# Kernel optimization log

Measured on AMD Instinct MI355X. Metric: run time of the kernel, lower is better.

Reference implementation:

```python
import jax, jax.numpy as jnp
import numpy as np

EPS = 1e-5  # torch BatchNorm default eps


def _bn_relu(x, g, b, relu):
    # Training-mode BatchNorm1d over (N, C, L): stats over axes (0, 2).
    m = jnp.mean(x, axis=(0, 2), keepdims=True)
    v = jnp.var(x, axis=(0, 2), keepdims=True)
    y = (x - m) * jax.lax.rsqrt(v + EPS) * g[None, :, None] + b[None, :, None]
    return jax.nn.relu(y) if relu else y


def setup_inputs() -> dict:
    key = jax.random.key(0)
    k0, k1, k2 = jax.random.split(key, 3)
    N, C, H = 256, 512, 64  # batch, channels (inplanes==planes), spatial positions (mask_channel)
    x = jax.random.normal(k0, (N, C, H), dtype=jnp.float32)
    # LocallyConnected2d weights: torch shape (1, out, in, H, 1, k^2=1) -> (out, in, H)
    w1 = jax.random.normal(k1, (C, C, H), dtype=jnp.float32) * 0.02
    w2 = jax.random.normal(k2, (C, C, H), dtype=jnp.float32) * 0.02
    g1 = jnp.ones((C,), jnp.float32)
    b1 = jnp.zeros((C,), jnp.float32)
    g2 = jnp.ones((C,), jnp.float32)
    b2 = jnp.zeros((C,), jnp.float32)
    return {"x": x, "w1": w1, "g1": g1, "b1": b1, "w2": w2, "g2": g2, "b2": b2}


def reference(x, w1, g1, b1, w2, g2, b2):
    # conv1: locally-connected 1x1 -> per-position matmul over channels
    out = jnp.einsum('nch,och->noh', x, w1)          # (N, C, H)
    out = _bn_relu(out, g1, b1, relu=True)
    # conv2
    out = jnp.einsum('nch,och->noh', out, w2)
    out = _bn_relu(out, g2, b2, relu=False)
    # residual add (downsample is None) + final relu
    return jax.nn.relu(out + x)
```

## Files before the change

kernel.cpp:

```cpp
#include <hip/hip_runtime.h>

typedef float  f32x4  __attribute__((ext_vector_type(4)));
typedef __bf16 bf16x8 __attribute__((ext_vector_type(8)));
typedef __bf16 bf16x4 __attribute__((ext_vector_type(4)));
typedef __bf16 bf16x2 __attribute__((ext_vector_type(2)));

#define N_ 256
#define C_ 512
#define H_ 64

__global__ __launch_bounds__(256) void k_prep(const float* __restrict__ x,
                                              const float* __restrict__ w1,
                                              const float* __restrict__ w2,
                                              __bf16* __restrict__ xT,
                                              __bf16* __restrict__ w1T,
                                              __bf16* __restrict__ w2T,
                                              float* __restrict__ stats) {
  __shared__ float tile[64][65];
  const int by = blockIdx.y;
  const int t  = threadIdx.x;
  if (by == 0 && blockIdx.x == 0) {
#pragma unroll
    for (int i = 0; i < 8; ++i) stats[i * 256 + t] = 0.f;
  }
  const float* src;
  __bf16* dst;
  int p, P;
  if (by < 256)      { src = x;  dst = xT;  p = by;       P = 256; }
  else if (by < 768) { src = w1; dst = w1T; p = by - 256; P = 512; }
  else               { src = w2; dst = w2T; p = by - 768; P = 512; }
  const int q0 = blockIdx.x * 64;
  const float* s = src + ((size_t)p * 512 + q0) * 64;
  const int a = t >> 4, b = t & 15;
#pragma unroll
  for (int j = 0; j < 4; ++j) {
    const int qq = j * 16 + a;
    const float4 v = *reinterpret_cast<const float4*>(s + qq * 64 + b * 4);
    tile[qq][b * 4 + 0] = v.x;
    tile[qq][b * 4 + 1] = v.y;
    tile[qq][b * 4 + 2] = v.z;
    tile[qq][b * 4 + 3] = v.w;
  }
  __syncthreads();
#pragma unroll
  for (int j = 0; j < 4; ++j) {
    const int hh = j * 16 + a;
    bf16x4 y;
#pragma unroll
    for (int e = 0; e < 4; ++e) y[e] = (__bf16)tile[b * 4 + e][hh];
    *reinterpret_cast<bf16x4*>(dst + ((size_t)hh * P + p) * 512 + q0 + b * 4) = y;
  }
}

template <bool BN_A>
__global__ __launch_bounds__(256, 2) void k_gemm(
    const __bf16* __restrict__ A,
    const __bf16* __restrict__ B,
    __bf16* __restrict__ Co,
    const float* __restrict__ sum_in, const float* __restrict__ sq_in,
    const float* __restrict__ g, const float* __restrict__ bb,
    float* __restrict__ sum_out, float* __restrict__ sq_out) {
  const int wkid = (blockIdx.x & 7) * 64 + (blockIdx.x >> 3);
  const int h  = wkid >> 3;
  const int tm = (wkid >> 2) & 1, tn = wkid & 3;
  const int m0 = tm * 128, n0 = tn * 128;
  const __bf16* Ah = A + ((size_t)h * N_ + m0) * C_;
  const __bf16* Bh = B + ((size_t)h * C_ + n0) * C_;
  __shared__ __bf16 As[2][128 * 64];
  __shared__ __bf16 Bs[2][128 * 64];
  __shared__ float a_lds[512], c_lds[512];
  const int tid  = threadIdx.x;
  const int lane = tid & 63, wid = tid >> 6;
  const int wr = wid >> 1, wc = wid & 1;
  const int lrow8 = lane >> 3;
  const int swz   = (lane & 7) ^ lrow8;

  if (BN_A) {
#pragma unroll
    for (int ch = tid; ch < 512; ch += 256) {
      const float m    = sum_in[ch] * (1.f / 16384.f);
      const float var  = fmaxf(0.f, sq_in[ch] * (1.f / 16384.f) - m * m);
      const float aa   = g[ch] * rsqrtf(var + 1e-5f);
      a_lds[ch] = aa;
      c_lds[ch] = bb[ch] - m * aa;
    }
    __syncthreads();
  }

  auto stage_b = [&](int buf, int kt) {
#pragma unroll
    for (int i = 0; i < 4; ++i) {
      const int rbase = wid * 32 + i * 8;
      const __bf16* gb = Bh + (size_t)(rbase + lrow8) * C_ + kt * 64 + swz * 8;
      __builtin_amdgcn_global_load_lds(
          (const __attribute__((address_space(1))) void*)gb,
          (__attribute__((address_space(3))) void*)(&Bs[buf][rbase * 64]), 16, 0, 0);
    }
  };
  auto stage_a = [&](int buf, int kt) {
#pragma unroll
    for (int i = 0; i < 4; ++i) {
      const int rbase = wid * 32 + i * 8;
      const __bf16* ga = Ah + (size_t)(rbase + lrow8) * C_ + kt * 64 + swz * 8;
      __builtin_amdgcn_global_load_lds(
          (const __attribute__((address_space(1))) void*)ga,
          (__attribute__((address_space(3))) void*)(&As[buf][rbase * 64]), 16, 0, 0);
    }
  };
  const int lr32 = tid >> 3, cch = tid & 7;
  auto load_a = [&](bf16x8* v, int kt) {
#pragma unroll
    for (int i = 0; i < 4; ++i)
      v[i] = *reinterpret_cast<const bf16x8*>(
          Ah + (size_t)(i * 32 + lr32) * C_ + kt * 64 + cch * 8);
  };
  auto bn_write = [&](const bf16x8* v, int buf, int kt) {
    const int cg = kt * 64 + cch * 8;
    const f32x4 s0 = *reinterpret_cast<const f32x4*>(&a_lds[cg]);
    const f32x4 s1 = *reinterpret_cast<const f32x4*>(&a_lds[cg + 4]);
    const f32x4 h0 = *reinterpret_cast<const f32x4*>(&c_lds[cg]);
    const f32x4 h1 = *reinterpret_cast<const f32x4*>(&c_lds[cg + 4]);
#pragma unroll
    for (int i = 0; i < 4; ++i) {
      const int row = i * 32 + lr32;
      bf16x8 y;
#pragma unroll
      for (int e = 0; e < 4; ++e) {
        y[e]     = (__bf16)fmaxf(0.f, fmaf((float)v[i][e],     s0[e], h0[e]));
        y[e + 4] = (__bf16)fmaxf(0.f, fmaf((float)v[i][e + 4], s1[e], h1[e]));
      }
      const int boff = row * 128 + ((cch * 16) ^ ((row & 7) << 4));
      *reinterpret_cast<bf16x8*>(reinterpret_cast<char*>(&As[buf][0]) + boff) = y;
    }
  };

  f32x4 acc[4][4] = {};
  const int fr = lane & 15, kc = lane >> 4;
  auto compute = [&](int buf) {
#pragma unroll
    for (int kk = 0; kk < 2; ++kk) {
      bf16x8 af[4], bfq[4];
#pragma unroll
      for (int mf = 0; mf < 4; ++mf) {
        const int row  = wr * 64 + mf * 16 + fr;
        const int boff = row * 128 + (((kk * 64 + kc * 16)) ^ ((row & 7) << 4));
        af[mf] = *reinterpret_cast<const bf16x8*>(
            reinterpret_cast<const char*>(&As[buf][0]) + boff);
      }
#pragma unroll
      for (int nf = 0; nf < 4; ++nf) {
        const int row  = wc * 64 + nf * 16 + fr;
        const int boff = row * 128 + (((kk * 64 + kc * 16)) ^ ((row & 7) << 4));
        bfq[nf] = *reinterpret_cast<const bf16x8*>(
            reinterpret_cast<const char*>(&Bs[buf][0]) + boff);
      }
#pragma unroll
      for (int mf = 0; mf < 4; ++mf)
#pragma unroll
        for (int nf = 0; nf < 4; ++nf)
          acc[mf][nf] = __builtin_amdgcn_mfma_f32_16x16x32_bf16(af[mf], bfq[nf], acc[mf][nf], 0, 0, 0);
    }
  };

  if (BN_A) {
    bf16x8 v0[4];
    load_a(v0, 0);
    bn_write(v0, 0, 0);
  } else {
    stage_a(0, 0);
  }
  stage_b(0, 0);
  __syncthreads();

  int buf = 0;
  for (int kt = 0; kt < 8; ++kt) {
    bf16x8 vn[4];
    if (kt < 7) {
      stage_b(buf ^ 1, kt + 1);
      if (!BN_A) stage_a(buf ^ 1, kt + 1);
      else       load_a(vn, kt + 1);
    }
    compute(buf);
    if (BN_A && kt < 7) bn_write(vn, buf ^ 1, kt + 1);
    __syncthreads();
    buf ^= 1;
  }

  const int rq = (lane >> 4) * 4;
  __bf16* Ch = Co + (size_t)h * N_ * C_;
#pragma unroll
  for (int nf = 0; nf < 4; ++nf) {
    const int oc = n0 + wc * 64 + nf * 16 + fr;
    float s = 0.f, s2 = 0.f;
#pragma unroll
    for (int mf = 0; mf < 4; ++mf) {
      const int rb = m0 + wr * 64 + mf * 16 + rq;
      f32x4 v = acc[mf][nf];
#pragma unroll
      for (int j = 0; j < 4; ++j) {
        const float f = v[j];
        Ch[(size_t)(rb + j) * C_ + oc] = (__bf16)f;
        s += f;
        s2 += f * f;
      }
    }
    s  += __shfl_xor(s, 16);  s  += __shfl_xor(s, 32);
    s2 += __shfl_xor(s2, 16); s2 += __shfl_xor(s2, 32);
    if (lane < 16) {
      atomicAdd(&sum_out[oc], s);
      atomicAdd(&sq_out[oc], s2);
    }
  }
}

__global__ __launch_bounds__(256) void k_finalize(const __bf16* __restrict__ t2,
                                                  const float* __restrict__ x,
                                                  const float* __restrict__ sum2,
                                                  const float* __restrict__ sq2,
                                                  const float* __restrict__ g2,
                                                  const float* __restrict__ b2,
                                                  float* __restrict__ out) {
  __shared__ float tile[64][65];
  __shared__ float a2s[64], c2s[64];
  const int n  = blockIdx.y;
  const int o0 = blockIdx.x * 64;
  const int t  = threadIdx.x;
  if (t < 64) {
    const int o = o0 + t;
    const float m    = sum2[o] * (1.f / 16384.f);
    const float var  = fmaxf(0.f, sq2[o] * (1.f / 16384.f) - m * m);
    const float a    = g2[o] * rsqrtf(var + 1e-5f);
    a2s[t] = a;
    c2s[t] = b2[o] - m * a;
  }
#pragma unroll
  for (int j = 0; j < 8; ++j) {
    const int hh = j * 8 + (t >> 5);
    const int ol = (t & 31) * 2;
    bf16x2 v = *reinterpret_cast<const bf16x2*>(t2 + ((size_t)hh * N_ + n) * C_ + o0 + ol);
    tile[hh][ol]     = (float)v[0];
    tile[hh][ol + 1] = (float)v[1];
  }
  __syncthreads();
  const int ol = t >> 2;
  const int hb = (t & 3) * 16;
  const int o  = o0 + ol;
  const float a = a2s[ol], c = c2s[ol];
  const float4* xp = reinterpret_cast<const float4*>(x + ((size_t)n * C_ + o) * H_ + hb);
  float4* op = reinterpret_cast<float4*>(out + ((size_t)n * C_ + o) * H_ + hb);
#pragma unroll
  for (int i4 = 0; i4 < 4; ++i4) {
    const float4 xv = xp[i4];
    float4 r;
    r.x = fmaxf(0.f, fmaf(a, tile[hb + i4 * 4 + 0][ol], c) + xv.x);
    r.y = fmaxf(0.f, fmaf(a, tile[hb + i4 * 4 + 1][ol], c) + xv.y);
    r.z = fmaxf(0.f, fmaf(a, tile[hb + i4 * 4 + 2][ol], c) + xv.z);
    r.w = fmaxf(0.f, fmaf(a, tile[hb + i4 * 4 + 3][ol], c) + xv.w);
    op[i4] = r;
  }
}

extern "C" void kernel_launch(void* const* d_in, const int* in_sizes, int n_in,
                              void* d_out, int out_size, void* d_ws, size_t ws_size,
                              hipStream_t stream) {
  const float* x  = (const float*)d_in[0];
  const float* w1 = (const float*)d_in[1];
  const float* g1 = (const float*)d_in[2];
  const float* b1 = (const float*)d_in[3];
  const float* w2 = (const float*)d_in[4];
  const float* g2 = (const float*)d_in[5];
  const float* b2 = (const float*)d_in[6];
  float* out = (float*)d_out;

  char* ws = (char*)d_ws;
  float* stats = (float*)ws;
  float* sum1 = stats,        *sq1 = stats + 512;
  float* sum2 = stats + 1024, *sq2 = stats + 1536;
  const size_t MB = (size_t)1 << 20;
  __bf16* xT  = (__bf16*)(ws + 64 * 1024);
  __bf16* w1T = (__bf16*)(ws + 64 * 1024 + 16 * MB);
  __bf16* w2T = (__bf16*)(ws + 64 * 1024 + 48 * MB);
  __bf16* t1T = (__bf16*)(ws + 64 * 1024 + 80 * MB);
  __bf16* t2T = (__bf16*)(ws + 64 * 1024 + 96 * MB);

  k_prep<<<dim3(8, 1280), 256, 0, stream>>>(x, w1, w2, xT, w1T, w2T, stats);

  k_gemm<false><<<512, 256, 0, stream>>>(xT, w1T, t1T, nullptr, nullptr,
                                         nullptr, nullptr, sum1, sq1);
  k_gemm<true><<<512, 256, 0, stream>>>(t1T, w2T, t2T, sum1, sq1, g1, b1,
                                        sum2, sq2);

  k_finalize<<<dim3(8, 256), 256, 0, stream>>>(t2T, x, sum2, sq2, g2, b2, out);
}
```

Measured before the change: 104.4 us.

## Switch intermediates to row-major (row, h, c) layout with wider prep transposes

Intermediate bf16 buffers change from an h-major [H][rows][C] layout to a [rows][H*C] layout with row stride 32768. The prep kernel's writes become contiguous per source row, and it now handles 256 channels per block, packing bf16 pairs in LDS and writing 16-byte vectors. The GEMM loads and stores use the new strided addressing, and the finalize kernel reads 4-wide bf16 vectors. The aim is more coalesced, wider memory traffic in prep and finalize. The cost is that GEMM tiles now stride 64 KB between rows, which may hurt DRAM/TLB locality.

```diff
diff --git a/kernel.cpp b/kernel.cpp
--- a/kernel.cpp
+++ b/kernel.cpp
@@ -1,13 +1,20 @@
 #include <hip/hip_runtime.h>
+#include <stdint.h>
 
 typedef float  f32x4  __attribute__((ext_vector_type(4)));
 typedef __bf16 bf16x8 __attribute__((ext_vector_type(8)));
 typedef __bf16 bf16x4 __attribute__((ext_vector_type(4)));
-typedef __bf16 bf16x2 __attribute__((ext_vector_type(2)));
 
 #define N_ 256
 #define C_ 512
 #define H_ 64
+#define RS_ 32768
+
+__device__ __forceinline__ uint32_t pack_bf16x2(float a, float b) {
+  const uint16_t ua = __builtin_bit_cast(uint16_t, (__bf16)a);
+  const uint16_t ub = __builtin_bit_cast(uint16_t, (__bf16)b);
+  return (uint32_t)ua | ((uint32_t)ub << 16);
+}
 
 __global__ __launch_bounds__(256) void k_prep(const float* __restrict__ x,
                                               const float* __restrict__ w1,
@@ -16,39 +23,51 @@
                                               __bf16* __restrict__ w1T,
                                               __bf16* __restrict__ w2T,
                                               float* __restrict__ stats) {
-  __shared__ float tile[64][65];
+  __shared__ uint32_t tile[256][33];
+  const int t  = threadIdx.x;
   const int by = blockIdx.y;
-  const int t  = threadIdx.x;
   if (by == 0 && blockIdx.x == 0) {
 #pragma unroll
     for (int i = 0; i < 8; ++i) stats[i * 256 + t] = 0.f;
   }
   const float* src;
   __bf16* dst;
-  int p, P;
-  if (by < 256)      { src = x;  dst = xT;  p = by;       P = 256; }
-  else if (by < 768) { src = w1; dst = w1T; p = by - 256; P = 512; }
-  else               { src = w2; dst = w2T; p = by - 768; P = 512; }
-  const int q0 = blockIdx.x * 64;
-  const float* s = src + ((size_t)p * 512 + q0) * 64;
-  const int a = t >> 4, b = t & 15;
-#pragma unroll
-  for (int j = 0; j < 4; ++j) {
-    const int qq = j * 16 + a;
-    const float4 v = *reinterpret_cast<const float4*>(s + qq * 64 + b * 4);
-    tile[qq][b * 4 + 0] = v.x;
-    tile[qq][b * 4 + 1] = v.y;
-    tile[qq][b * 4 + 2] = v.z;
-    tile[qq][b * 4 + 3] = v.w;
+  int p;
+  if (by < 256)      { src = x;  dst = xT;  p = by; }
+  else if (by < 768) { src = w1; dst = w1T; p = by - 256; }
+  else               { src = w2; dst = w2T; p = by - 768; }
+  const int ch0 = blockIdx.x * 256;
+  const float* sbase = src + ((size_t)p * 512 + ch0) * 64;
+
+#pragma unroll
+  for (int j = 0; j < 16; ++j) {
+    const int fidx = j * 256 + t;
+    const int c = fidx >> 4, hq = fidx & 15;
+    const float4 v = *reinterpret_cast<const float4*>(sbase + c * 64 + hq * 4);
+    tile[c][hq * 2]     = pack_bf16x2(v.x, v.y);
+    tile[c][hq * 2 + 1] = pack_bf16x2(v.z, v.w);
   }
   __syncthreads();
-#pragma unroll
-  for (int j = 0; j < 4; ++j) {
-    const int hh = j * 16 + a;
-    bf16x4 y;
-#pragma unroll
-    for (int e = 0; e < 4; ++e) y[e] = (__bf16)tile[b * 4 + e][hh];
-    *reinterpret_cast<bf16x4*>(dst + ((size_t)hh * P + p) * 512 + q0 + b * 4) = y;
+
+  __bf16* dbase = dst + (size_t)p * RS_ + ch0;
+#pragma unroll
+  for (int j = 0; j < 8; ++j) {
+    const int ci = j * 256 + t;
+    const int cb = ci & 31, h = ci >> 5;
+    const int hm = h >> 1;
+    const bool odd = (h & 1) != 0;
+    uint32_t W[8];
+#pragma unroll
+    for (int i = 0; i < 8; ++i) W[i] = tile[cb * 8 + i][hm];
+    uint4 o;
+    uint32_t* op = reinterpret_cast<uint32_t*>(&o);
+#pragma unroll
+    for (int k = 0; k < 4; ++k) {
+      const uint32_t wa = W[2 * k], wb = W[2 * k + 1];
+      op[k] = odd ? ((wa >> 16) | (wb & 0xFFFF0000u))
+                  : ((wa & 0xFFFFu) | (wb << 16));
+    }
+    *reinterpret_cast<uint4*>(dbase + (size_t)h * 512 + cb * 8) = o;
   }
 }
 
@@ -64,8 +83,8 @@
   const int h  = wkid >> 3;
   const int tm = (wkid >> 2) & 1, tn = wkid & 3;
   const int m0 = tm * 128, n0 = tn * 128;
-  const __bf16* Ah = A + ((size_t)h * N_ + m0) * C_;
-  const __bf16* Bh = B + ((size_t)h * C_ + n0) * C_;
+  const __bf16* Ah = A + (size_t)m0 * RS_ + (size_t)h * C_;
+  const __bf16* Bh = B + (size_t)n0 * RS_ + (size_t)h * C_;
   __shared__ __bf16 As[2][128 * 64];
   __shared__ __bf16 Bs[2][128 * 64];
   __shared__ float a_lds[512], c_lds[512];
@@ -91,7 +110,7 @@
 #pragma unroll
     for (int i = 0; i < 4; ++i) {
       const int rbase = wid * 32 + i * 8;
-      const __bf16* gb = Bh + (size_t)(rbase + lrow8) * C_ + kt * 64 + swz * 8;
+      const __bf16* gb = Bh + (size_t)(rbase + lrow8) * RS_ + kt * 64 + swz * 8;
       __builtin_amdgcn_global_load_lds(
           (const __attribute__((address_space(1))) void*)gb,
           (__attribute__((address_space(3))) void*)(&Bs[buf][rbase * 64]), 16, 0, 0);
@@ -101,7 +120,7 @@
 #pragma unroll
     for (int i = 0; i < 4; ++i) {
       const int rbase = wid * 32 + i * 8;
-      const __bf16* ga = Ah + (size_t)(rbase + lrow8) * C_ + kt * 64 + swz * 8;
+      const __bf16* ga = Ah + (size_t)(rbase + lrow8) * RS_ + kt * 64 + swz * 8;
       __builtin_amdgcn_global_load_lds(
           (const __attribute__((address_space(1))) void*)ga,
           (__attribute__((address_space(3))) void*)(&As[buf][rbase * 64]), 16, 0, 0);
@@ -112,7 +131,7 @@
 #pragma unroll
     for (int i = 0; i < 4; ++i)
       v[i] = *reinterpret_cast<const bf16x8*>(
-          Ah + (size_t)(i * 32 + lr32) * C_ + kt * 64 + cch * 8);
+          Ah + (size_t)(i * 32 + lr32) * RS_ + kt * 64 + cch * 8);
   };
   auto bn_write = [&](const bf16x8* v, int buf, int kt) {
     const int cg = kt * 64 + cch * 8;
@@ -143,14 +162,14 @@
 #pragma unroll
       for (int mf = 0; mf < 4; ++mf) {
         const int row  = wr * 64 + mf * 16 + fr;
-        const int boff = row * 128 + (((kk * 64 + kc * 16)) ^ ((row & 7) << 4));
+        const int boff = row * 128 + ((kk * 64 + kc * 16) ^ ((row & 7) << 4));
         af[mf] = *reinterpret_cast<const bf16x8*>(
             reinterpret_cast<const char*>(&As[buf][0]) + boff);
       }
 #pragma unroll
       for (int nf = 0; nf < 4; ++nf) {
         const int row  = wc * 64 + nf * 16 + fr;
-        const int boff = row * 128 + (((kk * 64 + kc * 16)) ^ ((row & 7) << 4));
+        const int boff = row * 128 + ((kk * 64 + kc * 16) ^ ((row & 7) << 4));
         bfq[nf] = *reinterpret_cast<const bf16x8*>(
             reinterpret_cast<const char*>(&Bs[buf][0]) + boff);
       }
@@ -187,7 +206,6 @@
   }
 
   const int rq = (lane >> 4) * 4;
-  __bf16* Ch = Co + (size_t)h * N_ * C_;
 #pragma unroll
   for (int nf = 0; nf < 4; ++nf) {
     const int oc = n0 + wc * 64 + nf * 16 + fr;
@@ -199,7 +217,7 @@
 #pragma unroll
       for (int j = 0; j < 4; ++j) {
         const float f = v[j];
-        Ch[(size_t)(rb + j) * C_ + oc] = (__bf16)f;
+        Co[(size_t)(rb + j) * RS_ + (size_t)h * C_ + oc] = (__bf16)f;
         s += f;
         s2 += f * f;
       }
@@ -233,13 +251,14 @@
     a2s[t] = a;
     c2s[t] = b2[o] - m * a;
   }
-#pragma unroll
-  for (int j = 0; j < 8; ++j) {
-    const int hh = j * 8 + (t >> 5);
-    const int ol = (t & 31) * 2;
-    bf16x2 v = *reinterpret_cast<const bf16x2*>(t2 + ((size_t)hh * N_ + n) * C_ + o0 + ol);
-    tile[hh][ol]     = (float)v[0];
-    tile[hh][ol + 1] = (float)v[1];
+  const __bf16* tb = t2 + (size_t)n * RS_ + o0;
+#pragma unroll
+  for (int j = 0; j < 4; ++j) {
+    const int hh = j * 16 + (t >> 4);
+    const int ol = (t & 15) * 4;
+    const bf16x4 v = *reinterpret_cast<const bf16x4*>(tb + (size_t)hh * 512 + ol);
+#pragma unroll
+    for (int e = 0; e < 4; ++e) tile[hh][ol + e] = (float)v[e];
   }
   __syncthreads();
   const int ol = t >> 2;
@@ -283,7 +302,7 @@
   __bf16* t1T = (__bf16*)(ws + 64 * 1024 + 80 * MB);
   __bf16* t2T = (__bf16*)(ws + 64 * 1024 + 96 * MB);
 
-  k_prep<<<dim3(8, 1280), 256, 0, stream>>>(x, w1, w2, xT, w1T, w2T, stats);
+  k_prep<<<dim3(2, 1280), 256, 0, stream>>>(x, w1, w2, xT, w1T, w2T, stats);
 
   k_gemm<false><<<512, 256, 0, stream>>>(xT, w1T, t1T, nullptr, nullptr,
                                          nullptr, nullptr, sum1, sq1);
```

Result: slower. 107.7 us (+3.2%).
